# Optimization experiments

Measured on AMD Instinct MI355X. Metric: run time of the kernel, lower is better.

## Reference

```python
import jax, jax.numpy as jnp
import numpy as np

B, K, DIM = 8192, 256, 1024


def setup_inputs() -> dict:
    key = jax.random.key(0)
    k1, k2, k3 = jax.random.split(key, 3)
    x = jax.random.normal(k1, (B, DIM), dtype=jnp.float32)
    centers = jax.random.uniform(k2, (K, DIM), dtype=jnp.float32)
    # torch init: D = 0.2 * rand + 0.9
    D = 0.2 * jax.random.uniform(k3, (K, DIM), dtype=jnp.float32) + 0.9
    return {"x": x, "centers": centers, "D": D}


def reference(x, centers, D):
    # Per-class axis-aligned (diagonal) covariance
    D_abs = jnp.abs(D) + 1e-4                      # [K, DIM]
    D_inv = 1.0 / D_abs                            # [K, DIM]
    log_det = jnp.sum(jnp.log(D_abs), axis=1)      # [K]
    det_scale_factor = -0.5 * log_det
    det_scale_safe = jnp.exp(det_scale_factor - jnp.max(det_scale_factor))  # [K]

    # dist_sq[b,k] = sum_d (x[b,d]-c[k,d])^2 * D_inv[k,d]
    # Expanded quadratic form avoids materializing the [B,K,DIM] diff tensor.
    x2 = jnp.einsum('bd,kd->bk', x * x, D_inv)             # [B, K]
    xc = jnp.einsum('bd,kd->bk', x, centers * D_inv)       # [B, K]
    c2 = jnp.sum(centers * centers * D_inv, axis=1)        # [K]
    dist_sq = x2 - 2.0 * xc + c2[None, :]                  # [B, K]

    # Gaussian path (isCauchy=False)
    expo = -0.5 * dist_sq
    expo_safe = expo - jnp.max(expo, axis=-1, keepdims=True)
    numer_safe = det_scale_safe[None, :] * jnp.exp(expo_safe)
    denom_safe = jnp.sum(numer_safe, axis=1, keepdims=True)
    resp = numer_safe / denom_safe                         # [B, K]
    return resp
```

## Files before the change

### kernel.cpp

```cpp
#include <hip/hip_runtime.h>

typedef _Float16 f16x8 __attribute__((ext_vector_type(8)));
typedef _Float16 f16x4 __attribute__((ext_vector_type(4)));
typedef float f32x4 __attribute__((ext_vector_type(4)));

#define B_N 8192
#define K_N 256
#define DIM_N 1024

__global__ __launch_bounds__(256) void prep_w(const float* __restrict__ Dm,
                                              const float* __restrict__ Cm,
                                              _Float16* __restrict__ Upk,
                                              _Float16* __restrict__ Wpk,
                                              float* __restrict__ ec) {
    const int k = blockIdx.x, t = threadIdx.x;
    const int d = t * 4;
    const float4 dv = *(const float4*)(Dm + (size_t)k * DIM_N + d);
    const float4 cv = *(const float4*)(Cm + (size_t)k * DIM_N + d);
    float dd[4] = {dv.x, dv.y, dv.z, dv.w};
    float cc[4] = {cv.x, cv.y, cv.z, cv.w};
    f16x4 uo, wo;
    float llog = 0.f, lc2 = 0.f;
#pragma unroll
    for (int i = 0; i < 4; ++i) {
        float da = fabsf(dd[i]) + 1e-4f;
        float dinv = 1.0f / da;
        llog += logf(da);
        lc2 += cc[i] * cc[i] * dinv;
        uo[i] = (_Float16)(dinv - 1.0f);
        wo[i] = (_Float16)(-2.0f * cc[i] * dinv);
    }
    const int cg = k >> 4, cl = k & 15;
    const int kc = d >> 5, g = (d >> 3) & 3, j0 = d & 7;
    const size_t off = ((size_t)(cg * 32 + kc) * 64 + g * 16 + cl) * 8 + j0;
    *(f16x4*)(Upk + off) = uo;
    *(f16x4*)(Wpk + off) = wo;
    float both = llog + lc2;
#pragma unroll
    for (int m = 1; m <= 32; m <<= 1) both += __shfl_xor(both, m, 64);
    __shared__ float sb[4];
    if ((t & 63) == 0) sb[t >> 6] = both;
    __syncthreads();
    if (t == 0) ec[k] = -0.5f * (sb[0] + sb[1] + sb[2] + sb[3]);
}

__global__ __launch_bounds__(512, 1)
void gmm_fused(const float* __restrict__ x,
               const _Float16* __restrict__ Upk,
               const _Float16* __restrict__ Wpk,
               const float* __restrict__ ecg,
               float* __restrict__ out) {
    __shared__ __align__(16) char lds[32768];
    __shared__ float red[8][32];

    const int tid = threadIdx.x;
    const int wave = tid >> 6, lane = tid & 63;
    const int l15 = lane & 15, g4 = lane >> 4;
    const int bRow = blockIdx.x * 32;

    const int srow = tid >> 4, sdg = tid & 15;
    const float* xp = x + (size_t)(bRow + srow) * DIM_N + sdg * 4;
    const int wByte = srow * 128 + ((((sdg >> 1) ^ (srow & 7)) << 4) | ((sdg & 1) << 3));

    const _Float16* upb = Upk + (size_t)(wave * 2) * 32 * 512 + lane * 8;
    const _Float16* wpb = Wpk + (size_t)(wave * 2) * 32 * 512 + lane * 8;

    int aRd[2][2];
#pragma unroll
    for (int m = 0; m < 2; ++m)
#pragma unroll
        for (int k2 = 0; k2 < 2; ++k2) {
            const int row = m * 16 + l15;
            aRd[m][k2] = row * 128 + ((((k2 * 4 + g4) ^ (row & 7)) << 4));
        }

    f32x4 acc[2][2];
#pragma unroll
    for (int m = 0; m < 2; ++m)
#pragma unroll
        for (int n = 0; n < 2; ++n) { f32x4 z = {0.f, 0.f, 0.f, 0.f}; acc[m][n] = z; }

    float4 xv[6];
    f16x8 ub[2][2][2], wb[2][2][2];

    auto issueX = [&](int slot, int c) { xv[slot] = *(const float4*)(xp + c * 64); };
    auto issueB = [&](int bank, int c) {
#pragma unroll
        for (int n = 0; n < 2; ++n)
#pragma unroll
            for (int k2 = 0; k2 < 2; ++k2) {
                const int kc = c * 2 + k2;
                ub[bank][n][k2] = *(const f16x8*)(upb + (size_t)(n * 32 + kc) * 512);
                wb[bank][n][k2] = *(const f16x8*)(wpb + (size_t)(n * 32 + kc) * 512);
            }
    };
    auto stage1 = [&](int buf, int sub, int slot) {
        char* base = lds + buf * 16384 + sub * 4096;
        const float f0 = xv[slot].x, f1 = xv[slot].y, f2 = xv[slot].z, f3 = xv[slot].w;
        f16x4 h2 = {(_Float16)(f0 * f0), (_Float16)(f1 * f1),
                    (_Float16)(f2 * f2), (_Float16)(f3 * f3)};
        f16x4 hx = {(_Float16)f0, (_Float16)f1, (_Float16)f2, (_Float16)f3};
        *(f16x4*)(base + wByte) = h2;
        *(f16x4*)(base + 8192 + wByte) = hx;
    };
    auto compute = [&](int buf, int sub, int bank) {
        char* base = lds + buf * 16384 + sub * 4096;
        f16x8 a2f[2][2], axf[2][2];
#pragma unroll
        for (int m = 0; m < 2; ++m)
#pragma unroll
            for (int k2 = 0; k2 < 2; ++k2) {
                a2f[m][k2] = *(const f16x8*)(base + aRd[m][k2]);
                axf[m][k2] = *(const f16x8*)(base + 8192 + aRd[m][k2]);
            }
#pragma unroll
        for (int m = 0; m < 2; ++m)
#pragma unroll
            for (int n = 0; n < 2; ++n)
#pragma unroll
                for (int k2 = 0; k2 < 2; ++k2) {
                    acc[m][n] = __builtin_amdgcn_mfma_f32_16x16x32_f16(a2f[m][k2], ub[bank][n][k2], acc[m][n], 0, 0, 0);
                    acc[m][n] = __builtin_amdgcn_mfma_f32_16x16x32_f16(axf[m][k2], wb[bank][n][k2], acc[m][n], 0, 0, 0);
                }
    };

    issueB(0, 0);
    issueB(1, 1);
#pragma unroll
    for (int s = 0; s < 6; ++s) issueX(s, s);
    stage1(0, 0, 0);
    stage1(0, 1, 1);
    asm volatile("s_waitcnt lgkmcnt(0)" ::: "memory");
    __builtin_amdgcn_s_barrier();
    __builtin_amdgcn_sched_barrier(0);

#pragma unroll
    for (int p = 0; p < 8; ++p) {
        const int buf = p & 1, nbuf = buf ^ 1;
        if (p < 5) { issueX((2 * p) % 6, 2 * p + 6); issueX((2 * p + 1) % 6, 2 * p + 7); }
        if (p < 7) { stage1(nbuf, 0, (2 * p + 2) % 6); stage1(nbuf, 1, (2 * p + 3) % 6); }
        compute(buf, 0, 0);
        if (p < 7) issueB(0, 2 * p + 2);
        compute(buf, 1, 1);
        if (p < 7) issueB(1, 2 * p + 3);
        if (p < 7) {
            asm volatile("s_waitcnt lgkmcnt(0)" ::: "memory");
            __builtin_amdgcn_s_barrier();
            __builtin_amdgcn_sched_barrier(0);
        }
    }

    const int cls0 = wave * 32 + l15;
    const float ecv[2] = {ecg[cls0], ecg[cls0 + 16]};

    float e[2][2][4];
#pragma unroll
    for (int m = 0; m < 2; ++m)
#pragma unroll
        for (int n = 0; n < 2; ++n)
#pragma unroll
            for (int j = 0; j < 4; ++j)
                e[m][n][j] = fmaf(-0.5f, acc[m][n][j], ecv[n]);

    float mx[2][4];
#pragma unroll
    for (int m = 0; m < 2; ++m)
#pragma unroll
        for (int j = 0; j < 4; ++j) mx[m][j] = fmaxf(e[m][0][j], e[m][1][j]);
#pragma unroll
    for (int msk = 1; msk <= 8; msk <<= 1)
#pragma unroll
        for (int m = 0; m < 2; ++m)
#pragma unroll
            for (int j = 0; j < 4; ++j)
                mx[m][j] = fmaxf(mx[m][j], __shfl_xor(mx[m][j], msk, 64));
    if (l15 == 0) {
#pragma unroll
        for (int m = 0; m < 2; ++m)
#pragma unroll
            for (int j = 0; j < 4; ++j) red[wave][m * 16 + g4 * 4 + j] = mx[m][j];
    }
    __syncthreads();
    float gm[2][4];
#pragma unroll
    for (int m = 0; m < 2; ++m)
#pragma unroll
        for (int j = 0; j < 4; ++j) {
            const int r = m * 16 + g4 * 4 + j;
            float v = red[0][r];
#pragma unroll
            for (int w = 1; w < 8; ++w) v = fmaxf(v, red[w][r]);
            gm[m][j] = v;
        }
    __syncthreads();

    float p2[2][2][4], sm[2][4];
#pragma unroll
    for (int m = 0; m < 2; ++m)
#pragma unroll
        for (int j = 0; j < 4; ++j) sm[m][j] = 0.f;
#pragma unroll
    for (int m = 0; m < 2; ++m)
#pragma unroll
        for (int n = 0; n < 2; ++n)
#pragma unroll
            for (int j = 0; j < 4; ++j) {
                p2[m][n][j] = __expf(e[m][n][j] - gm[m][j]);
                sm[m][j] += p2[m][n][j];
            }
#pragma unroll
    for (int msk = 1; msk <= 8; msk <<= 1)
#pragma unroll
        for (int m = 0; m < 2; ++m)
#pragma unroll
            for (int j = 0; j < 4; ++j) sm[m][j] += __shfl_xor(sm[m][j], msk, 64);
    if (l15 == 0) {
#pragma unroll
        for (int m = 0; m < 2; ++m)
#pragma unroll
            for (int j = 0; j < 4; ++j) red[wave][m * 16 + g4 * 4 + j] = sm[m][j];
    }
    __syncthreads();
#pragma unroll
    for (int m = 0; m < 2; ++m)
#pragma unroll
        for (int j = 0; j < 4; ++j) {
            const int r = m * 16 + g4 * 4 + j;
            float t = red[0][r];
#pragma unroll
            for (int w = 1; w < 8; ++w) t += red[w][r];
            const float inv = 1.0f / t;
#pragma unroll
            for (int n = 0; n < 2; ++n)
                out[(size_t)(bRow + r) * K_N + cls0 + n * 16] = p2[m][n][j] * inv;
        }
}

extern "C" void kernel_launch(void* const* d_in, const int* in_sizes, int n_in,
                              void* d_out, int out_size, void* d_ws, size_t ws_size,
                              hipStream_t stream) {
    const float* x = (const float*)d_in[0];
    const float* cen = (const float*)d_in[1];
    const float* Dm = (const float*)d_in[2];
    float* out = (float*)d_out;

    char* ws = (char*)d_ws;
    _Float16* Upk = (_Float16*)(ws);
    _Float16* Wpk = (_Float16*)(ws + 524288);
    float* ec = (float*)(ws + 1048576);

    prep_w<<<dim3(K_N), dim3(256), 0, stream>>>(Dm, cen, Upk, Wpk, ec);
    gmm_fused<<<dim3(B_N / 32), dim3(512), 0, stream>>>(x, Upk, Wpk, ec, out);
}
```

Before: 30.67 us.

## Stage whole x tile in LDS once and square it in registers

The x tile for the block is now converted to fp16 and written once into a 64KB LDS buffer in quarter chunks, where before x and x² went into a double-buffered 32KB area. x² is recomputed from the loaded fp16 x fragment at MFMA time, which halves LDS writes and space per element. The schedule moves from 8 barrier-synchronised phases to 4, and MFMA sections run at raised wave priority via s_setprio. The trade-offs are that x² is now formed by squaring an fp16 value, which changes rounding, and that the larger LDS footprint may limit occupancy.

```diff
diff --git a/kernel.cpp b/kernel.cpp
--- a/kernel.cpp
+++ b/kernel.cpp
@@ -50,7 +50,7 @@
                const _Float16* __restrict__ Wpk,
                const float* __restrict__ ecg,
                float* __restrict__ out) {
-    __shared__ __align__(16) char lds[32768];
+    __shared__ __align__(16) char xlds[65536];
     __shared__ float red[8][32];
 
     const int tid = threadIdx.x;
@@ -58,32 +58,40 @@
     const int l15 = lane & 15, g4 = lane >> 4;
     const int bRow = blockIdx.x * 32;
 
-    const int srow = tid >> 4, sdg = tid & 15;
-    const float* xp = x + (size_t)(bRow + srow) * DIM_N + sdg * 4;
-    const int wByte = srow * 128 + ((((sdg >> 1) ^ (srow & 7)) << 4) | ((sdg & 1) << 3));
+    const int srow = tid >> 4, sd = (tid & 15) * 4;
+    const float* xq = x + (size_t)(bRow + srow) * DIM_N + sd;
+    int wB[4];
+#pragma unroll
+    for (int j = 0; j < 4; ++j) {
+        const int slot = (sd >> 3) + 8 * j;
+        wB[j] = srow * 512 + (((slot ^ (srow & 7)) << 4) | ((sd & 4) << 1));
+    }
 
     const _Float16* upb = Upk + (size_t)(wave * 2) * 32 * 512 + lane * 8;
     const _Float16* wpb = Wpk + (size_t)(wave * 2) * 32 * 512 + lane * 8;
 
-    int aRd[2][2];
-#pragma unroll
-    for (int m = 0; m < 2; ++m)
-#pragma unroll
-        for (int k2 = 0; k2 < 2; ++k2) {
-            const int row = m * 16 + l15;
-            aRd[m][k2] = row * 128 + ((((k2 * 4 + g4) ^ (row & 7)) << 4));
+    f32x4 acc[2][2];
+#pragma unroll
+    for (int m = 0; m < 2; ++m)
+#pragma unroll
+        for (int n = 0; n < 2; ++n) { f32x4 z = {0.f, 0.f, 0.f, 0.f}; acc[m][n] = z; }
+
+    float4 xs[2][4];
+    f16x8 ub[2][2][2], wb[2][2][2];
+
+    auto issueQ = [&](int bank, int q) {
+#pragma unroll
+        for (int j = 0; j < 4; ++j) xs[bank][j] = *(const float4*)(xq + q * 256 + j * 64);
+    };
+    auto writeQ = [&](int bank, int q) {
+        char* base = xlds + q * 16384;
+#pragma unroll
+        for (int j = 0; j < 4; ++j) {
+            const float4 v = xs[bank][j];
+            f16x4 h = {(_Float16)v.x, (_Float16)v.y, (_Float16)v.z, (_Float16)v.w};
+            *(f16x4*)(base + wB[j]) = h;
         }
-
-    f32x4 acc[2][2];
-#pragma unroll
-    for (int m = 0; m < 2; ++m)
-#pragma unroll
-        for (int n = 0; n < 2; ++n) { f32x4 z = {0.f, 0.f, 0.f, 0.f}; acc[m][n] = z; }
-
-    float4 xv[6];
-    f16x8 ub[2][2][2], wb[2][2][2];
-
-    auto issueX = [&](int slot, int c) { xv[slot] = *(const float4*)(xp + c * 64); };
+    };
     auto issueB = [&](int bank, int c) {
 #pragma unroll
         for (int n = 0; n < 2; ++n)
@@ -94,25 +102,20 @@
                 wb[bank][n][k2] = *(const f16x8*)(wpb + (size_t)(n * 32 + kc) * 512);
             }
     };
-    auto stage1 = [&](int buf, int sub, int slot) {
-        char* base = lds + buf * 16384 + sub * 4096;
-        const float f0 = xv[slot].x, f1 = xv[slot].y, f2 = xv[slot].z, f3 = xv[slot].w;
-        f16x4 h2 = {(_Float16)(f0 * f0), (_Float16)(f1 * f1),
-                    (_Float16)(f2 * f2), (_Float16)(f3 * f3)};
-        f16x4 hx = {(_Float16)f0, (_Float16)f1, (_Float16)f2, (_Float16)f3};
-        *(f16x4*)(base + wByte) = h2;
-        *(f16x4*)(base + 8192 + wByte) = hx;
-    };
-    auto compute = [&](int buf, int sub, int bank) {
-        char* base = lds + buf * 16384 + sub * 4096;
-        f16x8 a2f[2][2], axf[2][2];
+    auto compute = [&](int c, int bank) {
+        const char* base = xlds + (c >> 2) * 16384;
+        const int cl = c & 3;
+        f16x8 axf[2][2], a2f[2][2];
 #pragma unroll
         for (int m = 0; m < 2; ++m)
 #pragma unroll
             for (int k2 = 0; k2 < 2; ++k2) {
-                a2f[m][k2] = *(const f16x8*)(base + aRd[m][k2]);
-                axf[m][k2] = *(const f16x8*)(base + 8192 + aRd[m][k2]);
+                const int row = m * 16 + l15;
+                const int slot = cl * 8 + k2 * 4 + g4;
+                axf[m][k2] = *(const f16x8*)(base + row * 512 + (((slot ^ (l15 & 7)) << 4)));
+                a2f[m][k2] = axf[m][k2] * axf[m][k2];
             }
+        __builtin_amdgcn_s_setprio(1);
 #pragma unroll
         for (int m = 0; m < 2; ++m)
 #pragma unroll
@@ -122,33 +125,45 @@
                     acc[m][n] = __builtin_amdgcn_mfma_f32_16x16x32_f16(a2f[m][k2], ub[bank][n][k2], acc[m][n], 0, 0, 0);
                     acc[m][n] = __builtin_amdgcn_mfma_f32_16x16x32_f16(axf[m][k2], wb[bank][n][k2], acc[m][n], 0, 0, 0);
                 }
-    };
-
-    issueB(0, 0);
-    issueB(1, 1);
-#pragma unroll
-    for (int s = 0; s < 6; ++s) issueX(s, s);
-    stage1(0, 0, 0);
-    stage1(0, 1, 1);
-    asm volatile("s_waitcnt lgkmcnt(0)" ::: "memory");
-    __builtin_amdgcn_s_barrier();
-    __builtin_amdgcn_sched_barrier(0);
-
-#pragma unroll
-    for (int p = 0; p < 8; ++p) {
-        const int buf = p & 1, nbuf = buf ^ 1;
-        if (p < 5) { issueX((2 * p) % 6, 2 * p + 6); issueX((2 * p + 1) % 6, 2 * p + 7); }
-        if (p < 7) { stage1(nbuf, 0, (2 * p + 2) % 6); stage1(nbuf, 1, (2 * p + 3) % 6); }
-        compute(buf, 0, 0);
-        if (p < 7) issueB(0, 2 * p + 2);
-        compute(buf, 1, 1);
-        if (p < 7) issueB(1, 2 * p + 3);
-        if (p < 7) {
-            asm volatile("s_waitcnt lgkmcnt(0)" ::: "memory");
-            __builtin_amdgcn_s_barrier();
-            __builtin_amdgcn_sched_barrier(0);
-        }
-    }
+        __builtin_amdgcn_s_setprio(0);
+    };
+
+    issueB(0, 0); issueB(1, 1);
+    issueQ(0, 0); issueQ(1, 1);
+    writeQ(0, 0);
+    issueQ(0, 2);
+    asm volatile("s_waitcnt lgkmcnt(0)" ::: "memory");
+    __builtin_amdgcn_s_barrier();
+    __builtin_amdgcn_sched_barrier(0);
+    writeQ(1, 1);
+    issueQ(1, 3);
+    compute(0, 0); issueB(0, 2);
+    compute(1, 1); issueB(1, 3);
+    compute(2, 0); issueB(0, 4);
+    compute(3, 1); issueB(1, 5);
+    asm volatile("s_waitcnt lgkmcnt(0)" ::: "memory");
+    __builtin_amdgcn_s_barrier();
+    __builtin_amdgcn_sched_barrier(0);
+    writeQ(0, 2);
+    compute(4, 0); issueB(0, 6);
+    compute(5, 1); issueB(1, 7);
+    compute(6, 0); issueB(0, 8);
+    compute(7, 1); issueB(1, 9);
+    asm volatile("s_waitcnt lgkmcnt(0)" ::: "memory");
+    __builtin_amdgcn_s_barrier();
+    __builtin_amdgcn_sched_barrier(0);
+    writeQ(1, 3);
+    compute(8, 0);  issueB(0, 10);
+    compute(9, 1);  issueB(1, 11);
+    compute(10, 0); issueB(0, 12);
+    compute(11, 1); issueB(1, 13);
+    asm volatile("s_waitcnt lgkmcnt(0)" ::: "memory");
+    __builtin_amdgcn_s_barrier();
+    __builtin_amdgcn_sched_barrier(0);
+    compute(12, 0); issueB(0, 14);
+    compute(13, 1); issueB(1, 15);
+    compute(14, 0);
+    compute(15, 1);
 
     const int cls0 = wave * 32 + l15;
     const float ecv[2] = {ecg[cls0], ecg[cls0 + 16]};
```

Result: faster. 29.99 us (-2.2%).
